# Kernel tuning notes

Hardware: AMD Instinct MI355X
Metric: run time of the kernel (lower is better)

The kernel has to match this reference:

```python
import jax, jax.numpy as jnp
import numpy as np

GAMMA = 0.1   # soft-min temperature from __init__
BIG = 1e30    # finite stand-in for +inf (avoids inf-inf NaNs in logsumexp/grad)


def _soft_dtw(x, y, gamma):
    """Soft-DTW distance per batch element. x: (B,N,d), y: (B,M,d) -> (B,)."""
    B, N, _ = x.shape
    M = y.shape[1]
    # pairwise squared euclidean cost matrix, (B, N, M)
    D = (jnp.sum(x * x, -1)[:, :, None] + jnp.sum(y * y, -1)[:, None, :]
         - 2.0 * jnp.einsum('bnd,bmd->bnm', x, y))

    # Anti-diagonal DP: v_p[i] = R[i, p-i], vectors of length N+1 (i in 0..N).
    i_arr = jnp.arange(N + 1)
    ii = jnp.clip(i_arr - 1, 0, N - 1)
    pad = jnp.full((B, 1), BIG, D.dtype)

    def softmin(a, b, c):
        z = jnp.stack([a, b, c], 0) * (-1.0 / gamma)
        return -gamma * jax.scipy.special.logsumexp(z, axis=0)

    def step(carry, p):
        v2, v1 = carry  # diagonals p-2 and p-1, each (B, N+1)
        jj = jnp.clip(p - 1 - i_arr, 0, M - 1)
        d = D[:, ii, jj]                              # cost D[i-1, p-i-1]
        sh1 = jnp.concatenate([pad, v1[:, :-1]], 1)   # R[i-1, p-i]
        sh2 = jnp.concatenate([pad, v2[:, :-1]], 1)   # R[i-1, p-i-1]
        smin = softmin(sh1, v1, sh2)                  # v1 itself is R[i, p-i-1]
        valid = (i_arr >= 1) & (p - i_arr >= 1) & (p - i_arr <= M)
        v0 = jnp.where(valid[None, :], d + smin, BIG)
        return (v1, v0), None

    v0 = jnp.full((B, N + 1), BIG, D.dtype).at[:, 0].set(0.0)  # R[0,0]=0
    v1 = jnp.full((B, N + 1), BIG, D.dtype)                    # diag p=1 all inf
    (_, vlast), _ = jax.lax.scan(step, (v0, v1), jnp.arange(2, N + M + 1))
    return vlast[:, N]  # R[N, M]


def setup_inputs() -> dict:
    key = jax.random.key(0)
    kx, ky = jax.random.split(key)
    B, N, M, d = 64, 512, 512, 64
    # scaled down so exp(-softdtw) does not fully underflow
    x = 0.01 * jax.random.normal(kx, (B, N, d), jnp.float32)
    y = 0.01 * jax.random.normal(ky, (B, M, d), jnp.float32)
    return {"x": x, "y": y}


def reference(x, y):
    dist = _soft_dtw(x, y, GAMMA)          # (B,)
    w = jnp.exp(-dist)[:, None, None]      # (B,1,1)
    return x * w
```

## Files before the change

### kernel.cpp

```cpp
#include <hip/hip_runtime.h>
#include <hip/hip_bf16.h>

#define B_   64
#define N_   512
#define M_   512
#define Dm_  64
#define SINV 14.426950408889634f
#define LAG  16
#define RING 64
#define SPAD 1136
#define G_   71
#define T_EXP 24

#if __has_builtin(__builtin_amdgcn_exp2f)
#define EXP2F(x) __builtin_amdgcn_exp2f(x)
#else
#define EXP2F(x) exp2f(x)
#endif
#if __has_builtin(__builtin_amdgcn_logf)
#define LOG2F(x) __builtin_amdgcn_logf(x)
#else
#define LOG2F(x) __log2f(x)
#endif

#define EPOCH_BARRIER() asm volatile("s_waitcnt lgkmcnt(0)\n\ts_barrier" ::: "memory")

typedef __attribute__((ext_vector_type(8))) short bf8_t;
typedef __attribute__((ext_vector_type(4))) float f32x4;

static __device__ __forceinline__ ushort f2bf(float f) {
  uint u = __float_as_uint(f);
  u += 0x7fff + ((u >> 16) & 1);
  return (ushort)(u >> 16);
}

template <int CTRL>
static __device__ __forceinline__ float dppmaxf(float m) {
  const int i = __builtin_amdgcn_update_dpp(0, __float_as_int(m), CTRL, 0xF, 0xF, false);
  return fmaxf(m, __int_as_float(i));
}

__global__ __launch_bounds__(256) void dtw_dist_mfma(const float* __restrict__ x,
                                                     const float* __restrict__ y,
                                                     ushort* __restrict__ Ds) {
  __shared__ __align__(16) char ldsbuf[36864 + 1024];
  ushort* Xs = (ushort*)ldsbuf;
  ushort* Ys = (ushort*)(ldsbuf + 18432);
  ushort* SM = (ushort*)ldsbuf;
  float*  XN = (float*)(ldsbuf + 36864);
  float*  YN = (float*)(ldsbuf + 37376);

  const int b  = blockIdx.z;
  const int i0 = blockIdx.y * 128;
  const int j0 = blockIdx.x * 128;
  const int tid = threadIdx.x;

  {
    const int row = tid >> 1;
    const int hc  = (tid & 1) * 32;
    const float4* xr = (const float4*)(x + ((size_t)b * N_ + i0 + row) * Dm_ + hc);
    const float4* yr = (const float4*)(y + ((size_t)b * M_ + j0 + row) * Dm_ + hc);
    float sx = 0.f, sy = 0.f;
#pragma unroll
    for (int q = 0; q < 8; ++q) {
      float4 v = xr[q];
      sx += v.x * v.x + v.y * v.y + v.z * v.z + v.w * v.w;
      ushort4 h = make_ushort4(f2bf(v.x), f2bf(v.y), f2bf(v.z), f2bf(v.w));
      *(ushort4*)&Xs[row * 72 + hc + q * 4] = h;
      float4 u = yr[q];
      sy += u.x * u.x + u.y * u.y + u.z * u.z + u.w * u.w;
      ushort4 g = make_ushort4(f2bf(u.x), f2bf(u.y), f2bf(u.z), f2bf(u.w));
      *(ushort4*)&Ys[row * 72 + hc + q * 4] = g;
    }
    sx += __shfl_xor(sx, 1);
    sy += __shfl_xor(sy, 1);
    if (!(tid & 1)) { XN[row] = sx; YN[row] = sy; }
  }
  __syncthreads();

  const int w = tid >> 6, lane = tid & 63;
  const int wm = w >> 1, wn = w & 1;
  const int lr = lane & 15, lk = lane >> 4;

  f32x4 acc[4][4];
#pragma unroll
  for (int fm = 0; fm < 4; ++fm)
#pragma unroll
    for (int fn = 0; fn < 4; ++fn) acc[fm][fn] = (f32x4){0.f, 0.f, 0.f, 0.f};

#pragma unroll
  for (int kk2 = 0; kk2 < 2; ++kk2) {
    bf8_t a[4], bv[4];
#pragma unroll
    for (int f = 0; f < 4; ++f) {
      a[f]  = *(const bf8_t*)&Xs[(wm * 64 + f * 16 + lr) * 72 + kk2 * 32 + lk * 8];
      bv[f] = *(const bf8_t*)&Ys[(wn * 64 + f * 16 + lr) * 72 + kk2 * 32 + lk * 8];
    }
#pragma unroll
    for (int fm = 0; fm < 4; ++fm)
#pragma unroll
      for (int fn = 0; fn < 4; ++fn)
        acc[fm][fn] = __builtin_amdgcn_mfma_f32_16x16x32_bf16(a[fm], bv[fn],
                                                              acc[fm][fn], 0, 0, 0);
  }
  __syncthreads();

#pragma unroll
  for (int fm = 0; fm < 4; ++fm) {
#pragma unroll
    for (int q = 0; q < 4; ++q) {
      const int il = wm * 64 + fm * 16 + lk * 4 + q;
      const float xa = SINV * XN[il];
#pragma unroll
      for (int fn = 0; fn < 4; ++fn) {
        const int jl = wn * 64 + fn * 16 + lr;
        const float dp = xa + fmaf(-2.f * SINV, acc[fm][fn][q], SINV * YN[jl]);
        SM[il * 136 + jl] = f2bf(EXP2F(-dp));
      }
    }
  }
  __syncthreads();

  const int tt = tid >> 4;
  const int kk = tid & 15;
  ushort* gb = Ds + (size_t)b * G_ * N_ * 16;
#pragma unroll 1
  for (int tq = 0; tq < 8; ++tq) {
    const int Wq = (i0 >> 6) + (tq >> 2);
    const int Cq = i0 + tq * 16 + 16 * Wq + j0;
    const int t  = i0 + tq * 16 + tt;
    const int g0 = (Cq - 15) >> 4;
#pragma unroll 1
    for (int gg = 0; gg < 11; ++gg) {
      const int g = g0 + gg;
      const int c = 16 * g + kk - tt - Cq;
      if ((unsigned)c < 128u)
        gb[((size_t)g * N_ + t) * 16 + kk] = SM[(t - i0) * 136 + c];
    }
  }
}

template <int PH, int MODE>
__device__ __forceinline__ void dp_epoch8(const ushort* __restrict__ ldp,
                                          uint4 (&nxOld)[2], uint4 (&nxNew)[2],
                                          float (&dc)[16],
                                          float* ring, float (*wmax)[8],
                                          int rd_base, int wr_base, bool pub,
                                          int w, int lane, int offn,
                                          float& A, float& r, float& fprev, int& ktot) {
  constexpr bool EVEN = (PH & 1) == 0;
  constexpr bool TAIL = (MODE == 2);
  float f = 1.0f;
  if (EVEN) {
    const float4* wmp = (const float4*)wmax[PH == 0 ? 1 : 0];
    const float4 wa = wmp[0], wb = wmp[1];
    float bm = fmaxf(fmaxf(fmaxf(wa.x, wa.y), fmaxf(wa.z, wa.w)),
                     fmaxf(fmaxf(wb.x, wb.y), fmaxf(wb.z, wb.w)));
    int kE = T_EXP + 127 - (int)(__float_as_uint(bm) >> 23);
    kE = kE < -126 ? -126 : (kE > 126 ? 126 : kE);
    f = __uint_as_float((uint)(kE + 127) << 23);
    fprev = f; ktot += kE;
    A *= f; r *= f;
  }

  const float* rb = ring + rd_base;
  float rv0 = rb[(PH * 16 - 17) & (RING - 1)];
  const float4* rq = (const float4*)(rb + ((PH * 16 - 16) & (RING - 1)));
  float4 q0 = rq[0], q1 = rq[1], q2 = rq[2], q3 = rq[3];
  if (EVEN) {
    rv0 *= f;
    q0.x *= f; q0.y *= f; q0.z *= f; q0.w *= f;
    q1.x *= f; q1.y *= f; q1.z *= f; q1.w *= f;
    q2.x *= f; q2.y *= f; q2.z *= f; q2.w *= f;
    q3.x *= f; q3.y *= f; q3.z *= f;
  } else {
    rv0 *= fprev;
  }
  float rvk[16] = {rv0, q0.x, q0.y, q0.z, q0.w, q1.x, q1.y, q1.z,
                   q1.w, q2.x, q2.y, q2.z, q2.w, q3.x, q3.y, q3.z};

  if (MODE == 0) {
    const uint4* l4 = (const uint4*)ldp;
    nxNew[0] = l4[0];
    nxNew[1] = l4[1];
  }

  float rbuf[16];
  constexpr int KMAX = TAIL ? 15 : 16;
#pragma unroll
  for (int k = 0; k < KMAX; ++k) {
    const float pre = r + A;
    const int nbi = __builtin_amdgcn_update_dpp(__float_as_int(rvk[k]),
                    __float_as_int(r), 0x138 , 0xF, 0xF, false);
    const float nb = __int_as_float(nbi);
    A = nb;
    r = dc[k] * (pre + nb);
    rbuf[k] = r;
  }

  if (!TAIL) {
    if (!EVEN) {
      float m = rbuf[7];
      m = dppmaxf<0x111>(m); m = dppmaxf<0x112>(m);
      m = dppmaxf<0x114>(m); m = dppmaxf<0x118>(m);
      m = dppmaxf<0x142>(m); m = dppmaxf<0x143>(m);
      if (lane == 63) wmax[(PH >> 1) & 1][w] = m;
    }
    if (pub) {
      float4* wqp = (float4*)(ring + wr_base + PH * 16);
      wqp[0] = make_float4(rbuf[0], rbuf[1], rbuf[2], rbuf[3]);
      wqp[1] = make_float4(rbuf[4], rbuf[5], rbuf[6], rbuf[7]);
      wqp[2] = make_float4(rbuf[8], rbuf[9], rbuf[10], rbuf[11]);
      wqp[3] = make_float4(rbuf[12], rbuf[13], rbuf[14], rbuf[15]);
    }
    const uint us[8] = {nxOld[0].x, nxOld[0].y, nxOld[0].z, nxOld[0].w,
                        nxOld[1].x, nxOld[1].y, nxOld[1].z, nxOld[1].w};
#pragma unroll
    for (int p = 0; p < 8; ++p) {
      const float lo = __uint_as_float(us[p] << 16);
      const float hi = __uint_as_float(us[p] & 0xffff0000u);
      dc[2 * p]     = ((uint)(offn + 2 * p) < 512u) ? lo : 0.f;
      dc[2 * p + 1] = ((uint)(offn + 2 * p + 1) < 512u) ? hi : 0.f;
    }
    EPOCH_BARRIER();
  }
}

__global__ __launch_bounds__(512, 1) void dtw_dp8(const ushort* __restrict__ Ds,
                                                  const float* __restrict__ x,
                                                  float* __restrict__ out) {
  const int b    = blockIdx.x;
  const int t    = threadIdx.x;
  const int w    = t >> 6;
  const int lane = t & 63;
  const int skew = t + w * LAG;

  __shared__ __align__(16) float ring[8 * RING];
  __shared__ __align__(16) float wmax[2][8];
  __shared__ float wbc;
  ring[t] = 0.f;
  if (t < 16) wmax[t >> 3][t & 7] = __uint_as_float((uint)(T_EXP + 127) << 23);
  __syncthreads();

  const ushort* colp = Ds + ((size_t)b * G_ * N_ + t) * 16;
  const int rd_base = ((w + 7) & 7) * RING;
  const bool pub    = (lane == 63) && (w < 7);
  const int wr_base = w * RING;

  float A = (t == 0) ? 1.0f : 0.f;
  float r = 0.f;
  float fprev = 1.0f;
  int ktot = 0;

  uint4 bufA[2], bufB[2];
  {
    const uint4* l4 = (const uint4*)colp;
    bufA[0] = l4[0]; bufA[1] = l4[1];
    const uint4* l5 = (const uint4*)(colp + 8192);
    bufB[0] = l5[0]; bufB[1] = l5[1];
  }
  float dc[16];
  {
    const uint us[8] = {bufA[0].x, bufA[0].y, bufA[0].z, bufA[0].w,
                        bufA[1].x, bufA[1].y, bufA[1].z, bufA[1].w};
#pragma unroll
    for (int p = 0; p < 8; ++p) {
      const float lo = __uint_as_float(us[p] << 16);
      const float hi = __uint_as_float(us[p] & 0xffff0000u);
      dc[2 * p]     = ((uint)(2 * p - skew) < 512u) ? lo : 0.f;
      dc[2 * p + 1] = ((uint)(2 * p + 1 - skew) < 512u) ? hi : 0.f;
    }
  }

  const ushort* cr = colp + (size_t)2 * 8192;
  int offn = 16 - skew;
#pragma unroll 1
  for (int g = 0; g < 17; ++g) {
    dp_epoch8<0, 0>(cr, bufB, bufA, dc, ring, wmax, rd_base, wr_base, pub, w, lane, offn, A, r, fprev, ktot); cr += 8192; offn += 16;
    dp_epoch8<1, 0>(cr, bufA, bufB, dc, ring, wmax, rd_base, wr_base, pub, w, lane, offn, A, r, fprev, ktot); cr += 8192; offn += 16;
    dp_epoch8<2, 0>(cr, bufB, bufA, dc, ring, wmax, rd_base, wr_base, pub, w, lane, offn, A, r, fprev, ktot); cr += 8192; offn += 16;
    dp_epoch8<3, 0>(cr, bufA, bufB, dc, ring, wmax, rd_base, wr_base, pub, w, lane, offn, A, r, fprev, ktot); cr += 8192; offn += 16;
  }
  dp_epoch8<0, 0>(cr, bufB, bufA, dc, ring, wmax, rd_base, wr_base, pub, w, lane, offn, A, r, fprev, ktot); offn += 16;
  dp_epoch8<1, 1>(nullptr, bufA, bufB, dc, ring, wmax, rd_base, wr_base, pub, w, lane, offn, A, r, fprev, ktot);
  dp_epoch8<2, 2>(nullptr, bufB, bufA, dc, ring, wmax, rd_base, wr_base, pub, w, lane, offn, A, r, fprev, ktot);

  if (t == N_ - 1) wbc = EXP2F(0.1f * (LOG2F(r) - (float)ktot));
  __syncthreads();
  const float wsc = wbc;

  const float4* x4 = (const float4*)(x + (size_t)b * N_ * Dm_);
  float4* o4 = (float4*)(out + (size_t)b * N_ * Dm_);
#pragma unroll
  for (int e = 0; e < 16; ++e) {
    float4 v = x4[e * 512 + t];
    v.x *= wsc; v.y *= wsc; v.z *= wsc; v.w *= wsc;
    o4[e * 512 + t] = v;
  }
}

__global__ __launch_bounds__(512) void dtw_dp_fused(const float* __restrict__ x,
                                                    const float* __restrict__ y,
                                                    float* __restrict__ out) {
  __shared__ float v[3][516];
  const int b = blockIdx.x;
  const int t = threadIdx.x;
  const int i = t + 1;
  const float BIGF = 1e30f;
  if (t == 0) { v[0][0] = 0.f; v[1][0] = BIGF; v[2][0] = BIGF; }
  v[0][i] = BIGF;
  v[1][i] = BIGF;
  float xr[Dm_];
  const float* xrow = x + ((size_t)b * N_ + t) * Dm_;
#pragma unroll
  for (int k = 0; k < Dm_; ++k) xr[k] = xrow[k];
  __syncthreads();
  int cur = 2, m1 = 1, m2 = 0;
  const float GLN2 = 0.069314718055994531f;
  for (int p = 2; p <= N_ + M_; ++p) {
    const int j = p - i;
    const bool valid = (j >= 1) && (j <= M_);
    float d = 0.f;
    if (valid) {
      const float* yr = y + ((size_t)b * M_ + (j - 1)) * Dm_;
      float a = 0.f;
#pragma unroll
      for (int k = 0; k < Dm_; ++k) { float u = xr[k] - yr[k]; a = fmaf(u, u, a); }
      d = a;
    }
    const float a  = v[m1][i - 1];
    const float bb = v[m1][i];
    const float c  = v[m2][i - 1];
    const float mn = fminf(fminf(a, bb), c);
    const float s = exp2f((mn - a) * SINV) + exp2f((mn - bb) * SINV) +
                    exp2f((mn - c) * SINV);
    const float rr = valid ? (d + mn - GLN2 * log2f(s)) : BIGF;
    v[cur][i] = rr;
    if (t == 0) v[cur][0] = BIGF;
    __syncthreads();
    const int tmp = m2; m2 = m1; m1 = cur; cur = tmp;
  }
  const float dist = v[(N_ + M_) % 3][N_];
  const float wsc = expf(-dist);
  const float* xb = x + (size_t)b * N_ * Dm_;
  float* ob = out + (size_t)b * N_ * Dm_;
#pragma unroll
  for (int e = 0; e < (N_ * Dm_) / 512; ++e) {
    const int idx = e * 512 + t;
    ob[idx] = xb[idx] * wsc;
  }
}

extern "C" void kernel_launch(void* const* d_in, const int* in_sizes, int n_in,
                              void* d_out, int out_size, void* d_ws, size_t ws_size,
                              hipStream_t stream) {
  const float* x = (const float*)d_in[0];
  const float* y = (const float*)d_in[1];
  float* out = (float*)d_out;

  const size_t needS = (size_t)B_ * G_ * N_ * 16 * 2;

  if (ws_size >= needS) {
    ushort* Dsb = (ushort*)d_ws;
    dim3 g(M_ / 128, N_ / 128, B_);
    dtw_dist_mfma<<<g, dim3(256), 0, stream>>>(x, y, Dsb);
    dtw_dp8<<<dim3(B_), dim3(512), 0, stream>>>(Dsb, x, out);
  } else {
    dtw_dp_fused<<<dim3(B_), dim3(512), 0, stream>>>(x, y, out);
  }
}
```

Baseline: 87.64 us.

## Add dp9 wavefront DP with wider inter-wave skew and prefetched ring reads

```diff
diff --git a/kernel.cpp b/kernel.cpp
--- a/kernel.cpp
+++ b/kernel.cpp
@@ -6,11 +6,16 @@
 #define M_   512
 #define Dm_  64
 #define SINV 14.426950408889634f
+#define T_EXP 24
+
 #define LAG  16
 #define RING 64
 #define SPAD 1136
 #define G_   71
-#define T_EXP 24
+#define EXTRA2 32
+#define RING2  64
+#define SPAD2  1248
+#define G2     78
 
 #if __has_builtin(__builtin_amdgcn_exp2f)
 #define EXP2F(x) __builtin_amdgcn_exp2f(x)
@@ -40,6 +45,7 @@
   return fmaxf(m, __int_as_float(i));
 }
 
+template <int EX_, int GC_>
 __global__ __launch_bounds__(256) void dtw_dist_mfma(const float* __restrict__ x,
                                                      const float* __restrict__ y,
                                                      ushort* __restrict__ Ds) {
@@ -123,11 +129,11 @@
 
   const int tt = tid >> 4;
   const int kk = tid & 15;
-  ushort* gb = Ds + (size_t)b * G_ * N_ * 16;
+  ushort* gb = Ds + (size_t)b * GC_ * N_ * 16;
 #pragma unroll 1
   for (int tq = 0; tq < 8; ++tq) {
     const int Wq = (i0 >> 6) + (tq >> 2);
-    const int Cq = i0 + tq * 16 + 16 * Wq + j0;
+    const int Cq = i0 + tq * 16 + EX_ * Wq + j0;
     const int t  = i0 + tq * 16 + tt;
     const int g0 = (Cq - 15) >> 4;
 #pragma unroll 1
@@ -137,6 +143,167 @@
       if ((unsigned)c < 128u)
         gb[((size_t)g * N_ + t) * 16 + kk] = SM[(t - i0) * 136 + c];
     }
+  }
+}
+
+template <int PH, int MODE>
+__device__ __forceinline__ void dp_epoch9(const ushort* __restrict__ ldp,
+                                          uint4 (&nxOld)[2], uint4 (&nxNew)[2],
+                                          float (&dc)[16], float (&rvk)[16],
+                                          float* ring, float (*wmax)[8],
+                                          int rd_base, int wr_base, bool pub,
+                                          int w, int lane, int offn,
+                                          float& A, float& r,
+                                          float& fcur, float& fnext,
+                                          int& kEnext, int& ktot) {
+  constexpr bool ODD = (PH & 1) == 1;
+  constexpr bool TAIL = (MODE == 2);
+  if (ODD) {
+    A *= fnext; r *= fnext; ktot += kEnext; fcur = fnext;
+  }
+
+  if (MODE == 0) {
+    const uint4* l4 = (const uint4*)ldp;
+    nxNew[0] = l4[0]; nxNew[1] = l4[1];
+  }
+
+  float rbuf[16];
+  constexpr int KMAX = TAIL ? 15 : 16;
+#pragma unroll
+  for (int k = 0; k < KMAX; ++k) {
+    const float pre = r + A;
+    const int nbi = __builtin_amdgcn_update_dpp(__float_as_int(rvk[k]),
+                    __float_as_int(r), 0x138 , 0xF, 0xF, false);
+    const float nb = __int_as_float(nbi);
+    A = nb;
+    r = dc[k] * (pre + nb);
+    rbuf[k] = r;
+  }
+
+  if (!TAIL) {
+    if (ODD) {
+      float m = rbuf[7];
+      m = dppmaxf<0x111>(m); m = dppmaxf<0x112>(m);
+      m = dppmaxf<0x114>(m); m = dppmaxf<0x118>(m);
+      m = dppmaxf<0x142>(m); m = dppmaxf<0x143>(m);
+      if (lane == 63) wmax[(PH >> 1) & 1][w] = m;
+    } else {
+      const float4* wmp = (const float4*)wmax[PH == 0 ? 1 : 0];
+      const float4 wa = wmp[0], wb = wmp[1];
+      float bm = fmaxf(fmaxf(fmaxf(wa.x, wa.y), fmaxf(wa.z, wa.w)),
+                       fmaxf(fmaxf(wb.x, wb.y), fmaxf(wb.z, wb.w)));
+      int kE = T_EXP + 127 - (int)(__float_as_uint(bm) >> 23);
+      kE = kE < -126 ? -126 : (kE > 126 ? 126 : kE);
+      kEnext = kE;
+      fnext = __uint_as_float((uint)(kE + 127) << 23);
+    }
+    if (pub) {
+      float4* wqp = (float4*)(ring + wr_base + PH * 16);
+      wqp[0] = make_float4(rbuf[0], rbuf[1], rbuf[2], rbuf[3]);
+      wqp[1] = make_float4(rbuf[4], rbuf[5], rbuf[6], rbuf[7]);
+      wqp[2] = make_float4(rbuf[8], rbuf[9], rbuf[10], rbuf[11]);
+      wqp[3] = make_float4(rbuf[12], rbuf[13], rbuf[14], rbuf[15]);
+    }
+    {
+      constexpr int BQ = ((PH + 3) & 3) * 16;
+      const float* rb = ring + rd_base;
+      const float rv0 = rb[(BQ + 63) & 63];
+      const float4* rq = (const float4*)(rb + BQ);
+      const float4 q0 = rq[0], q1 = rq[1], q2 = rq[2], q3 = rq[3];
+      float s0, sk;
+      if (!ODD) { s0 = fcur * fnext; sk = fnext; }
+      else      { s0 = fcur;         sk = fcur;  }
+      rvk[0]  = rv0  * s0;
+      rvk[1]  = q0.x * sk; rvk[2]  = q0.y * sk; rvk[3]  = q0.z * sk; rvk[4]  = q0.w * sk;
+      rvk[5]  = q1.x * sk; rvk[6]  = q1.y * sk; rvk[7]  = q1.z * sk; rvk[8]  = q1.w * sk;
+      rvk[9]  = q2.x * sk; rvk[10] = q2.y * sk; rvk[11] = q2.z * sk; rvk[12] = q2.w * sk;
+      rvk[13] = q3.x * sk; rvk[14] = q3.y * sk; rvk[15] = q3.z * sk;
+    }
+    const uint us[8] = {nxOld[0].x, nxOld[0].y, nxOld[0].z, nxOld[0].w,
+                        nxOld[1].x, nxOld[1].y, nxOld[1].z, nxOld[1].w};
+#pragma unroll
+    for (int p = 0; p < 8; ++p) {
+      const float lo = __uint_as_float(us[p] << 16);
+      const float hi = __uint_as_float(us[p] & 0xffff0000u);
+      dc[2 * p]     = ((uint)(offn + 2 * p) < 512u) ? lo : 0.f;
+      dc[2 * p + 1] = ((uint)(offn + 2 * p + 1) < 512u) ? hi : 0.f;
+    }
+    EPOCH_BARRIER();
+  }
+}
+
+__global__ __launch_bounds__(512, 1) void dtw_dp9(const ushort* __restrict__ Ds,
+                                                  const float* __restrict__ x,
+                                                  float* __restrict__ out) {
+  const int b    = blockIdx.x;
+  const int t    = threadIdx.x;
+  const int w    = t >> 6;
+  const int lane = t & 63;
+  const int skew = t + w * EXTRA2;
+
+  __shared__ __align__(16) float ring[8 * RING2];
+  __shared__ __align__(16) float wmax[2][8];
+  __shared__ float wbc;
+  ring[t] = 0.f;
+  if (t < 16) wmax[t >> 3][t & 7] = __uint_as_float((uint)(T_EXP + 127) << 23);
+  __syncthreads();
+
+  const ushort* colp = Ds + ((size_t)b * G2 * N_ + t) * 16;
+  const int rd_base = ((w + 7) & 7) * RING2;
+  const bool pub    = (lane == 63) && (w < 7);
+  const int wr_base = w * RING2;
+
+  float A = (t == 0) ? 1.0f : 0.f;
+  float r = 0.f;
+  float fcur = 1.0f, fnext = 1.0f;
+  int kEnext = 0, ktot = 0;
+
+  uint4 bufA[2], bufB[2];
+  {
+    const uint4* l4 = (const uint4*)colp;
+    bufA[0] = l4[0]; bufA[1] = l4[1];
+    const uint4* l5 = (const uint4*)(colp + 8192);
+    bufB[0] = l5[0]; bufB[1] = l5[1];
+  }
+  float dc[16];
+  {
+    const uint us[8] = {bufA[0].x, bufA[0].y, bufA[0].z, bufA[0].w,
+                        bufA[1].x, bufA[1].y, bufA[1].z, bufA[1].w};
+#pragma unroll
+    for (int p = 0; p < 8; ++p) {
+      const float lo = __uint_as_float(us[p] << 16);
+      const float hi = __uint_as_float(us[p] & 0xffff0000u);
+      dc[2 * p]     = ((uint)(2 * p - skew) < 512u) ? lo : 0.f;
+      dc[2 * p + 1] = ((uint)(2 * p + 1 - skew) < 512u) ? hi : 0.f;
+    }
+  }
+  float rvk[16];
+#pragma unroll
+  for (int k = 0; k < 16; ++k) rvk[k] = 0.f;
+
+  const ushort* cr = colp + (size_t)2 * 8192;
+  int offn = 16 - skew;
+#pragma unroll 1
+  for (int g = 0; g < 19; ++g) {
+    dp_epoch9<0, 0>(cr, bufB, bufA, dc, rvk, ring, wmax, rd_base, wr_base, pub, w, lane, offn, A, r, fcur, fnext, kEnext, ktot); cr += 8192; offn += 16;
+    dp_epoch9<1, 0>(cr, bufA, bufB, dc, rvk, ring, wmax, rd_base, wr_base, pub, w, lane, offn, A, r, fcur, fnext, kEnext, ktot); cr += 8192; offn += 16;
+    dp_epoch9<2, 0>(cr, bufB, bufA, dc, rvk, ring, wmax, rd_base, wr_base, pub, w, lane, offn, A, r, fcur, fnext, kEnext, ktot); cr += 8192; offn += 16;
+    dp_epoch9<3, 0>(cr, bufA, bufB, dc, rvk, ring, wmax, rd_base, wr_base, pub, w, lane, offn, A, r, fcur, fnext, kEnext, ktot); cr += 8192; offn += 16;
+  }
+  dp_epoch9<0, 1>(nullptr, bufB, bufA, dc, rvk, ring, wmax, rd_base, wr_base, pub, w, lane, offn, A, r, fcur, fnext, kEnext, ktot);
+  dp_epoch9<1, 2>(nullptr, bufA, bufB, dc, rvk, ring, wmax, rd_base, wr_base, pub, w, lane, offn, A, r, fcur, fnext, kEnext, ktot);
+
+  if (t == N_ - 1) wbc = EXP2F(0.1f * (LOG2F(r) - (float)ktot));
+  __syncthreads();
+  const float wsc = wbc;
+
+  const float4* x4 = (const float4*)(x + (size_t)b * N_ * Dm_);
+  float4* o4 = (float4*)(out + (size_t)b * N_ * Dm_);
+#pragma unroll
+  for (int e = 0; e < 16; ++e) {
+    float4 v = x4[e * 512 + t];
+    v.x *= wsc; v.y *= wsc; v.z *= wsc; v.w *= wsc;
+    o4[e * 512 + t] = v;
   }
 }
 
@@ -191,7 +358,7 @@
   for (int k = 0; k < KMAX; ++k) {
     const float pre = r + A;
     const int nbi = __builtin_amdgcn_update_dpp(__float_as_int(rvk[k]),
-                    __float_as_int(r), 0x138 , 0xF, 0xF, false);
+                    __float_as_int(r), 0x138, 0xF, 0xF, false);
     const float nb = __int_as_float(nbi);
     A = nb;
     r = dc[k] * (pre + nb);
@@ -358,12 +525,17 @@
   const float* y = (const float*)d_in[1];
   float* out = (float*)d_out;
 
-  const size_t needS = (size_t)B_ * G_ * N_ * 16 * 2;
-
-  if (ws_size >= needS) {
+  const size_t need9 = (size_t)B_ * G2 * N_ * 16 * 2;
+  const size_t need8 = (size_t)B_ * G_ * N_ * 16 * 2;
+  dim3 g(M_ / 128, N_ / 128, B_);
+
+  if (ws_size >= need9) {
     ushort* Dsb = (ushort*)d_ws;
-    dim3 g(M_ / 128, N_ / 128, B_);
-    dtw_dist_mfma<<<g, dim3(256), 0, stream>>>(x, y, Dsb);
+    dtw_dist_mfma<EXTRA2, G2><<<g, dim3(256), 0, stream>>>(x, y, Dsb);
+    dtw_dp9<<<dim3(B_), dim3(512), 0, stream>>>(Dsb, x, out);
+  } else if (ws_size >= need8) {
+    ushort* Dsb = (ushort*)d_ws;
+    dtw_dist_mfma<LAG, G_><<<g, dim3(256), 0, stream>>>(x, y, Dsb);
     dtw_dp8<<<dim3(B_), dim3(512), 0, stream>>>(Dsb, x, out);
   } else {
     dtw_dp_fused<<<dim3(B_), dim3(512), 0, stream>>>(x, y, out);
```

New measurement: 94.36 us. +7.7%, slower.
